# Optimization experiments

Hardware: AMD Instinct MI355X
Metric: run time of the kernel (lower is better)

## Reference

```python
import jax, jax.numpy as jnp
import numpy as np

FFT_LEN = 256
BATCH = 65536


def _dft_kernels():
    n = np.arange(FFT_LEN)
    k = n.reshape(-1, 1)
    cos_k = np.cos(2 * np.pi * k * n / FFT_LEN).astype(np.float32)   # [K, N]
    sin_k = (-np.sin(2 * np.pi * k * n / FFT_LEN)).astype(np.float32)  # [K, N], note the minus sign
    return jnp.asarray(cos_k), jnp.asarray(sin_k)


def setup_inputs() -> dict:
    key = jax.random.key(0)
    x = jax.random.normal(key, (BATCH, 2, FFT_LEN), dtype=jnp.float32)
    cos_kernel, sin_kernel = _dft_kernels()
    return {"x": x, "cos_kernel": cos_kernel, "sin_kernel": sin_kernel}


def reference(x, cos_kernel, sin_kernel):
    # x: [B, 2, 256] -> real/imag channels. Conv1d(kernel=256, no pad) over L=256
    # is exactly a dense 256x256 matmul per channel (a direct O(n^2) DFT).
    x_real = x[:, 0, :]  # [B, 256]
    x_imag = x[:, 1, :]  # [B, 256]
    # real_conv(v) = cos_kernel @ v ; imag_conv(v) = sin_kernel @ v
    real_part = jnp.einsum('kn,bn->bk', cos_kernel, x_real) - jnp.einsum('kn,bn->bk', sin_kernel, x_imag)
    imag_part = jnp.einsum('kn,bn->bk', cos_kernel, x_imag) + jnp.einsum('kn,bn->bk', sin_kernel, x_real)
    out = jnp.concatenate([real_part, imag_part], axis=1)  # [B, 512]
    return out[:, :, None]  # [B, 512, 1] matches torch conv output length 1
```

## Files before the change

### kernel.cpp

```cpp
#include <hip/hip_runtime.h>
#include <hip/hip_bf16.h>
#include <stdint.h>


typedef __attribute__((ext_vector_type(8))) short bf16x8;
typedef __attribute__((ext_vector_type(4))) float f32x4;

#define KDIM 512
#define NDIM 512
#define BM 64

__device__ __forceinline__ ushort f2bf(float f) {
  union { float f; uint32_t u; } v; v.f = f;
  uint32_t r = (v.u + 0x7fffu + ((v.u >> 16) & 1u)) >> 16;
  return (ushort)r;
}

__global__ __launch_bounds__(512) void build_w_kernel(const float* __restrict__ cosk,
                                                      const float* __restrict__ sink,
                                                      ushort* __restrict__ Wf) {
  int g = blockIdx.x * 512 + threadIdx.x;
  int lane = g & 63;
  int nt = (g >> 6) & 31;
  int j = nt * 16 + (lane & 15);
  int kbase = (g >> 11) * 32 + (lane >> 4) * 8;
  bf16x8 w8;
#pragma unroll
  for (int e = 0; e < 8; ++e) {
    int k = kbase + e;
    float v;
    if (j < 256) {
      v = (k < 256) ? cosk[(j << 8) + k] : -sink[(j << 8) + (k - 256)];
    } else {
      int jj = j - 256;
      v = (k < 256) ? sink[(jj << 8) + k] : cosk[(jj << 8) + (k - 256)];
    }
    w8[e] = (short)f2bf(v);
  }
  *reinterpret_cast<bf16x8*>(Wf + (size_t)g * 8) = w8;
}

__device__ __forceinline__ bf16x8 cvt8(f32x4 a, f32x4 b) {
  bf16x8 w8;
  w8[0] = (short)f2bf(a[0]); w8[1] = (short)f2bf(a[1]);
  w8[2] = (short)f2bf(a[2]); w8[3] = (short)f2bf(a[3]);
  w8[4] = (short)f2bf(b[0]); w8[5] = (short)f2bf(b[1]);
  w8[6] = (short)f2bf(b[2]); w8[7] = (short)f2bf(b[3]);
  return w8;
}

__global__ __launch_bounds__(512) void dft_gemm_kernel(const float* __restrict__ A,
                                                       const ushort* __restrict__ Wf,
                                                       float* __restrict__ out) {
  __shared__ ushort As[2][BM * 64];

  const int tid  = threadIdx.x;
  const int lane = tid & 63;
  const int wid  = tid >> 6;
  const int m0   = blockIdx.x * BM;
  const int c0   = wid * 64;

  const int srow = tid >> 3;
  const int skq  = (tid & 7) * 8;
  const float* ap = A + (size_t)(m0 + srow) * KDIM + skq;
  const int swidx = (srow << 6) + (skq ^ ((srow & 7) << 3));

  const int lrow = lane & 15;
  const int lk8  = (lane >> 4) * 8;

  const ushort* wp = Wf + (size_t)(c0 >> 4) * 512 + lane * 8;

  f32x4 acc[4][4] = {};

  f32x4 q0 = *reinterpret_cast<const f32x4*>(ap);
  f32x4 q1 = *reinterpret_cast<const f32x4*>(ap + 4);
  f32x4 p0 = *reinterpret_cast<const f32x4*>(ap + 64);
  f32x4 p1 = *reinterpret_cast<const f32x4*>(ap + 68);
  *reinterpret_cast<bf16x8*>(&As[0][swidx]) = cvt8(q0, q1);
  asm volatile("s_waitcnt lgkmcnt(0)" ::: "memory");
  __builtin_amdgcn_s_barrier();

#pragma unroll
  for (int t = 0; t < 8; ++t) {
    if (t < 7)
      *reinterpret_cast<bf16x8*>(&As[(t + 1) & 1][swidx]) = cvt8(p0, p1);

    bf16x8 wfr[2][4];
#pragma unroll
    for (int kk = 0; kk < 2; ++kk)
#pragma unroll
      for (int mi = 0; mi < 4; ++mi)
        wfr[kk][mi] = *reinterpret_cast<const bf16x8*>(
            wp + (size_t)((t * 2 + kk) * 32 + mi) * 512);

    if (t < 6) {
      p0 = *reinterpret_cast<const f32x4*>(ap + (t + 2) * 64);
      p1 = *reinterpret_cast<const f32x4*>(ap + (t + 2) * 64 + 4);
    }

#pragma unroll
    for (int kk = 0; kk < 2; ++kk) {
      bf16x8 xfr[4];
#pragma unroll
      for (int ni = 0; ni < 4; ++ni) {
        int row = ni * 16 + lrow;
        int idx = (row << 6) + ((kk * 32 + lk8) ^ ((lrow & 7) << 3));
        xfr[ni] = *reinterpret_cast<const bf16x8*>(&As[t & 1][idx]);
      }
#pragma unroll
      for (int mi = 0; mi < 4; ++mi)
#pragma unroll
        for (int ni = 0; ni < 4; ++ni)
          acc[mi][ni] = __builtin_amdgcn_mfma_f32_16x16x32_bf16(
              wfr[kk][mi], xfr[ni], acc[mi][ni], 0, 0, 0);
    }

    if (t < 7) {
      asm volatile("s_waitcnt lgkmcnt(0)" ::: "memory");
      __builtin_amdgcn_s_barrier();
    }
  }

  const int jbase = c0 + (lane >> 4) * 4;
#pragma unroll
  for (int ni = 0; ni < 4; ++ni) {
    size_t rowb = (size_t)(m0 + ni * 16 + lrow) * NDIM;
#pragma unroll
    for (int mi = 0; mi < 4; ++mi)
      *reinterpret_cast<f32x4*>(out + rowb + jbase + mi * 16) = acc[mi][ni];
  }
}

extern "C" void kernel_launch(void* const* d_in, const int* in_sizes, int n_in,
                              void* d_out, int out_size, void* d_ws, size_t ws_size,
                              hipStream_t stream) {
  const float* x    = (const float*)d_in[0];
  const float* cosk = (const float*)d_in[1];
  const float* sink = (const float*)d_in[2];
  float* out = (float*)d_out;
  ushort* Wf = (ushort*)d_ws;

  build_w_kernel<<<64, 512, 0, stream>>>(cosk, sink, Wf);
  dft_gemm_kernel<<<65536 / BM, 512, 0, stream>>>(x, Wf, out);
}
```

Baseline: 72.74 us.

## Stage activations in two half-K LDS phases instead of a double-buffered loop

Replaces the 8-step double-buffered LDS pipeline with two phases. Each phase loads four K-slices of the input at once, converts them to bf16 into a larger LDS buffer, syncs once, then runs four MFMA steps. This cuts the per-step barriers from seven to two and puts more global loads in flight together. LDS use grows from 16KB to 64KB per block, and the added launch-bound hint of 4 blocks per CU may not be reachable at that LDS size. It also gives up overlapping the load of the second half with compute on the first.

```diff
diff --git a/kernel.cpp b/kernel.cpp
--- a/kernel.cpp
+++ b/kernel.cpp
@@ -49,10 +49,10 @@
   return w8;
 }
 
-__global__ __launch_bounds__(512) void dft_gemm_kernel(const float* __restrict__ A,
-                                                       const ushort* __restrict__ Wf,
-                                                       float* __restrict__ out) {
-  __shared__ ushort As[2][BM * 64];
+__global__ __launch_bounds__(512, 4) void dft_gemm_kernel(const float* __restrict__ A,
+                                                          const ushort* __restrict__ Wf,
+                                                          float* __restrict__ out) {
+  __shared__ ushort As[8][64 * 64];
 
   const int tid  = threadIdx.x;
   const int lane = tid & 63;
@@ -63,7 +63,7 @@
   const int srow = tid >> 3;
   const int skq  = (tid & 7) * 8;
   const float* ap = A + (size_t)(m0 + srow) * KDIM + skq;
-  const int swidx = (srow << 6) + (skq ^ ((srow & 7) << 3));
+  const int swb = (srow << 6) + (skq ^ ((srow & 7) << 3));
 
   const int lrow = lane & 15;
   const int lk8  = (lane >> 4) * 8;
@@ -72,19 +72,22 @@
 
   f32x4 acc[4][4] = {};
 
-  f32x4 q0 = *reinterpret_cast<const f32x4*>(ap);
-  f32x4 q1 = *reinterpret_cast<const f32x4*>(ap + 4);
-  f32x4 p0 = *reinterpret_cast<const f32x4*>(ap + 64);
-  f32x4 p1 = *reinterpret_cast<const f32x4*>(ap + 68);
-  *reinterpret_cast<bf16x8*>(&As[0][swidx]) = cvt8(q0, q1);
+  {
+    f32x4 s[8];
+#pragma unroll
+    for (int t = 0; t < 4; ++t) {
+      s[2 * t]     = *reinterpret_cast<const f32x4*>(ap + t * 64);
+      s[2 * t + 1] = *reinterpret_cast<const f32x4*>(ap + t * 64 + 4);
+    }
+#pragma unroll
+    for (int t = 0; t < 4; ++t)
+      *reinterpret_cast<bf16x8*>(&As[t][swb]) = cvt8(s[2 * t], s[2 * t + 1]);
+  }
   asm volatile("s_waitcnt lgkmcnt(0)" ::: "memory");
   __builtin_amdgcn_s_barrier();
 
 #pragma unroll
-  for (int t = 0; t < 8; ++t) {
-    if (t < 7)
-      *reinterpret_cast<bf16x8*>(&As[(t + 1) & 1][swidx]) = cvt8(p0, p1);
-
+  for (int t = 0; t < 4; ++t) {
     bf16x8 wfr[2][4];
 #pragma unroll
     for (int kk = 0; kk < 2; ++kk)
@@ -92,12 +95,6 @@
       for (int mi = 0; mi < 4; ++mi)
         wfr[kk][mi] = *reinterpret_cast<const bf16x8*>(
             wp + (size_t)((t * 2 + kk) * 32 + mi) * 512);
-
-    if (t < 6) {
-      p0 = *reinterpret_cast<const f32x4*>(ap + (t + 2) * 64);
-      p1 = *reinterpret_cast<const f32x4*>(ap + (t + 2) * 64 + 4);
-    }
-
 #pragma unroll
     for (int kk = 0; kk < 2; ++kk) {
       bf16x8 xfr[4];
@@ -105,7 +102,7 @@
       for (int ni = 0; ni < 4; ++ni) {
         int row = ni * 16 + lrow;
         int idx = (row << 6) + ((kk * 32 + lk8) ^ ((lrow & 7) << 3));
-        xfr[ni] = *reinterpret_cast<const bf16x8*>(&As[t & 1][idx]);
+        xfr[ni] = *reinterpret_cast<const bf16x8*>(&As[t][idx]);
       }
 #pragma unroll
       for (int mi = 0; mi < 4; ++mi)
@@ -114,10 +111,46 @@
           acc[mi][ni] = __builtin_amdgcn_mfma_f32_16x16x32_bf16(
               wfr[kk][mi], xfr[ni], acc[mi][ni], 0, 0, 0);
     }
+  }
 
-    if (t < 7) {
-      asm volatile("s_waitcnt lgkmcnt(0)" ::: "memory");
-      __builtin_amdgcn_s_barrier();
+  {
+    f32x4 s[8];
+#pragma unroll
+    for (int t = 0; t < 4; ++t) {
+      s[2 * t]     = *reinterpret_cast<const f32x4*>(ap + (4 + t) * 64);
+      s[2 * t + 1] = *reinterpret_cast<const f32x4*>(ap + (4 + t) * 64 + 4);
+    }
+#pragma unroll
+    for (int t = 0; t < 4; ++t)
+      *reinterpret_cast<bf16x8*>(&As[4 + t][swb]) = cvt8(s[2 * t], s[2 * t + 1]);
+  }
+  asm volatile("s_waitcnt lgkmcnt(0)" ::: "memory");
+  __builtin_amdgcn_s_barrier();
+
+#pragma unroll
+  for (int t = 4; t < 8; ++t) {
+    bf16x8 wfr[2][4];
+#pragma unroll
+    for (int kk = 0; kk < 2; ++kk)
+#pragma unroll
+      for (int mi = 0; mi < 4; ++mi)
+        wfr[kk][mi] = *reinterpret_cast<const bf16x8*>(
+            wp + (size_t)((t * 2 + kk) * 32 + mi) * 512);
+#pragma unroll
+    for (int kk = 0; kk < 2; ++kk) {
+      bf16x8 xfr[4];
+#pragma unroll
+      for (int ni = 0; ni < 4; ++ni) {
+        int row = ni * 16 + lrow;
+        int idx = (row << 6) + ((kk * 32 + lk8) ^ ((lrow & 7) << 3));
+        xfr[ni] = *reinterpret_cast<const bf16x8*>(&As[t][idx]);
+      }
+#pragma unroll
+      for (int mi = 0; mi < 4; ++mi)
+#pragma unroll
+        for (int ni = 0; ni < 4; ++ni)
+          acc[mi][ni] = __builtin_amdgcn_mfma_f32_16x16x32_bf16(
+              wfr[kk][mi], xfr[ni], acc[mi][ni], 0, 0, 0);
     }
   }
 
```

Result: no change. 72.25 us (-0.7%).

## Double block M tile to 128 rows and software-pipeline weight fragment loads

Applied to the files above, without the earlier changes.

The row tile grows from 64 to 128, so each weight fragment fetched from global memory is reused across twice as many MFMA tiles, which halves weight traffic per output. Each thread now stages 16 floats per row chunk, and the x prefetch is moved to the top of each iteration, with the LDS store delayed to the end of the iteration. Weight fragments for the next k-half are loaded while the current half computes. The accumulator count doubles to 32 f32x4 per thread with launch_bounds(512,2), which raises register pressure and risks spills or lower occupancy.

```diff
diff --git a/kernel.cpp b/kernel.cpp
--- a/kernel.cpp
+++ b/kernel.cpp
@@ -8,7 +8,7 @@
 
 #define KDIM 512
 #define NDIM 512
-#define BM 64
+#define BM 128
 
 __device__ __forceinline__ ushort f2bf(float f) {
   union { float f; uint32_t u; } v; v.f = f;
@@ -49,9 +49,9 @@
   return w8;
 }
 
-__global__ __launch_bounds__(512) void dft_gemm_kernel(const float* __restrict__ A,
-                                                       const ushort* __restrict__ Wf,
-                                                       float* __restrict__ out) {
+__global__ __launch_bounds__(512, 2) void dft_gemm_kernel(const float* __restrict__ A,
+                                                          const ushort* __restrict__ Wf,
+                                                          float* __restrict__ out) {
   __shared__ ushort As[2][BM * 64];
 
   const int tid  = threadIdx.x;
@@ -60,62 +60,94 @@
   const int m0   = blockIdx.x * BM;
   const int c0   = wid * 64;
 
-  const int srow = tid >> 3;
-  const int skq  = (tid & 7) * 8;
+  const int srow  = tid >> 2;
+  const int skq   = (tid & 3) * 16;
   const float* ap = A + (size_t)(m0 + srow) * KDIM + skq;
-  const int swidx = (srow << 6) + (skq ^ ((srow & 7) << 3));
+  const int slot0 = (tid & 3) * 2;
+  const int eA = srow * 64 + (((slot0)     ^ (srow & 7)) << 3);
+  const int eB = srow * 64 + (((slot0 + 1) ^ (srow & 7)) << 3);
 
   const int lrow = lane & 15;
   const int lk8  = (lane >> 4) * 8;
 
   const ushort* wp = Wf + (size_t)(c0 >> 4) * 512 + lane * 8;
 
-  f32x4 acc[4][4] = {};
+  f32x4 acc[4][8] = {};
 
-  f32x4 q0 = *reinterpret_cast<const f32x4*>(ap);
-  f32x4 q1 = *reinterpret_cast<const f32x4*>(ap + 4);
-  f32x4 p0 = *reinterpret_cast<const f32x4*>(ap + 64);
-  f32x4 p1 = *reinterpret_cast<const f32x4*>(ap + 68);
-  *reinterpret_cast<bf16x8*>(&As[0][swidx]) = cvt8(q0, q1);
+  {
+    f32x4 s0 = *reinterpret_cast<const f32x4*>(ap);
+    f32x4 s1 = *reinterpret_cast<const f32x4*>(ap + 4);
+    f32x4 s2 = *reinterpret_cast<const f32x4*>(ap + 8);
+    f32x4 s3 = *reinterpret_cast<const f32x4*>(ap + 12);
+    *reinterpret_cast<bf16x8*>(&As[0][eA]) = cvt8(s0, s1);
+    *reinterpret_cast<bf16x8*>(&As[0][eB]) = cvt8(s2, s3);
+  }
+  bf16x8 wcur[4];
+#pragma unroll
+  for (int mi = 0; mi < 4; ++mi)
+    wcur[mi] = *reinterpret_cast<const bf16x8*>(wp + (size_t)mi * 512);
   asm volatile("s_waitcnt lgkmcnt(0)" ::: "memory");
   __builtin_amdgcn_s_barrier();
 
 #pragma unroll
   for (int t = 0; t < 8; ++t) {
-    if (t < 7)
-      *reinterpret_cast<bf16x8*>(&As[(t + 1) & 1][swidx]) = cvt8(p0, p1);
-
-    bf16x8 wfr[2][4];
-#pragma unroll
-    for (int kk = 0; kk < 2; ++kk)
-#pragma unroll
-      for (int mi = 0; mi < 4; ++mi)
-        wfr[kk][mi] = *reinterpret_cast<const bf16x8*>(
-            wp + (size_t)((t * 2 + kk) * 32 + mi) * 512);
-
-    if (t < 6) {
-      p0 = *reinterpret_cast<const f32x4*>(ap + (t + 2) * 64);
-      p1 = *reinterpret_cast<const f32x4*>(ap + (t + 2) * 64 + 4);
+    f32x4 x0, x1, x2, x3;
+    if (t < 7) {
+      const float* apn = ap + (t + 1) * 64;
+      x0 = *reinterpret_cast<const f32x4*>(apn);
+      x1 = *reinterpret_cast<const f32x4*>(apn + 4);
+      x2 = *reinterpret_cast<const f32x4*>(apn + 8);
+      x3 = *reinterpret_cast<const f32x4*>(apn + 12);
     }
 
+    bf16x8 wnxt[4];
 #pragma unroll
-    for (int kk = 0; kk < 2; ++kk) {
-      bf16x8 xfr[4];
+    for (int mi = 0; mi < 4; ++mi)
+      wnxt[mi] = *reinterpret_cast<const bf16x8*>(
+          wp + (size_t)((t * 2 + 1) * 32 + mi) * 512);
+
+    {
+      bf16x8 xfr[8];
 #pragma unroll
-      for (int ni = 0; ni < 4; ++ni) {
+      for (int ni = 0; ni < 8; ++ni) {
         int row = ni * 16 + lrow;
-        int idx = (row << 6) + ((kk * 32 + lk8) ^ ((lrow & 7) << 3));
+        int idx = (row << 6) + (lk8 ^ ((lrow & 7) << 3));
         xfr[ni] = *reinterpret_cast<const bf16x8*>(&As[t & 1][idx]);
       }
 #pragma unroll
       for (int mi = 0; mi < 4; ++mi)
 #pragma unroll
-        for (int ni = 0; ni < 4; ++ni)
+        for (int ni = 0; ni < 8; ++ni)
           acc[mi][ni] = __builtin_amdgcn_mfma_f32_16x16x32_bf16(
-              wfr[kk][mi], xfr[ni], acc[mi][ni], 0, 0, 0);
+              wcur[mi], xfr[ni], acc[mi][ni], 0, 0, 0);
     }
 
     if (t < 7) {
+#pragma unroll
+      for (int mi = 0; mi < 4; ++mi)
+        wcur[mi] = *reinterpret_cast<const bf16x8*>(
+            wp + (size_t)((t * 2 + 2) * 32 + mi) * 512);
+    }
+
+    {
+      bf16x8 xfr[8];
+#pragma unroll
+      for (int ni = 0; ni < 8; ++ni) {
+        int row = ni * 16 + lrow;
+        int idx = (row << 6) + ((32 + lk8) ^ ((lrow & 7) << 3));
+        xfr[ni] = *reinterpret_cast<const bf16x8*>(&As[t & 1][idx]);
+      }
+#pragma unroll
+      for (int mi = 0; mi < 4; ++mi)
+#pragma unroll
+        for (int ni = 0; ni < 8; ++ni)
+          acc[mi][ni] = __builtin_amdgcn_mfma_f32_16x16x32_bf16(
+              wnxt[mi], xfr[ni], acc[mi][ni], 0, 0, 0);
+    }
+
+    if (t < 7) {
+      *reinterpret_cast<bf16x8*>(&As[(t + 1) & 1][eA]) = cvt8(x0, x1);
+      *reinterpret_cast<bf16x8*>(&As[(t + 1) & 1][eB]) = cvt8(x2, x3);
       asm volatile("s_waitcnt lgkmcnt(0)" ::: "memory");
       __builtin_amdgcn_s_barrier();
     }
@@ -123,7 +155,7 @@
 
   const int jbase = c0 + (lane >> 4) * 4;
 #pragma unroll
-  for (int ni = 0; ni < 4; ++ni) {
+  for (int ni = 0; ni < 8; ++ni) {
     size_t rowb = (size_t)(m0 + ni * 16 + lrow) * NDIM;
 #pragma unroll
     for (int mi = 0; mi < 4; ++mi)
```

New measurement: 70.24 us. 3.4% less time.

## Load fp32 input directly into LDS and convert to bf16 at fragment read

Applied to the files above, without the earlier changes.

Replaces the register-staged path (global load, bf16 convert, LDS store) with direct global-to-LDS loads of raw fp32 data into a triple-buffered, swizzled shared tile. Conversion to bf16 now happens when each wave reads its MFMA fragments. This removes register staging and the explicit LDS store, and lets loads run further ahead. The cost is double the LDS footprint and read bandwidth, and conversion work repeated across all eight waves. Inside the loop the barrier no longer has an explicit vmcnt wait, so correctness depends on the compiler inserting the right wait for the LDS DMA.

```diff
diff --git a/kernel.cpp b/kernel.cpp
--- a/kernel.cpp
+++ b/kernel.cpp
@@ -40,6 +40,12 @@
   *reinterpret_cast<bf16x8*>(Wf + (size_t)g * 8) = w8;
 }
 
+__device__ __forceinline__ void gload_lds16(const float* g, float* l) {
+  __builtin_amdgcn_global_load_lds(
+      (__attribute__((address_space(1))) const void*)g,
+      (__attribute__((address_space(3))) void*)l, 16, 0, 0);
+}
+
 __device__ __forceinline__ bf16x8 cvt8(f32x4 a, f32x4 b) {
   bf16x8 w8;
   w8[0] = (short)f2bf(a[0]); w8[1] = (short)f2bf(a[1]);
@@ -52,7 +58,7 @@
 __global__ __launch_bounds__(512) void dft_gemm_kernel(const float* __restrict__ A,
                                                        const ushort* __restrict__ Wf,
                                                        float* __restrict__ out) {
-  __shared__ ushort As[2][BM * 64];
+  __shared__ float Xs[3][BM * 64];
 
   const int tid  = threadIdx.x;
   const int lane = tid & 63;
@@ -60,31 +66,30 @@
   const int m0   = blockIdx.x * BM;
   const int c0   = wid * 64;
 
-  const int srow = tid >> 3;
-  const int skq  = (tid & 7) * 8;
-  const float* ap = A + (size_t)(m0 + srow) * KDIM + skq;
-  const int swidx = (srow << 6) + (skq ^ ((srow & 7) << 3));
+  const int r0 = wid * 8 + (lane >> 4);
+  const int r1 = r0 + 4;
+  const int slin = (lane & 15) >> 1;
+  const int h4   = (lane & 1) << 2;
+  const float* g0 = A + (size_t)(m0 + r0) * KDIM + (((slin ^ (r0 & 7)) << 3) + h4);
+  const float* g1 = A + (size_t)(m0 + r1) * KDIM + (((slin ^ (r1 & 7)) << 3) + h4);
 
   const int lrow = lane & 15;
-  const int lk8  = (lane >> 4) * 8;
+  const int g16  = lane >> 4;
 
   const ushort* wp = Wf + (size_t)(c0 >> 4) * 512 + lane * 8;
 
   f32x4 acc[4][4] = {};
 
-  f32x4 q0 = *reinterpret_cast<const f32x4*>(ap);
-  f32x4 q1 = *reinterpret_cast<const f32x4*>(ap + 4);
-  f32x4 p0 = *reinterpret_cast<const f32x4*>(ap + 64);
-  f32x4 p1 = *reinterpret_cast<const f32x4*>(ap + 68);
-  *reinterpret_cast<bf16x8*>(&As[0][swidx]) = cvt8(q0, q1);
-  asm volatile("s_waitcnt lgkmcnt(0)" ::: "memory");
+  gload_lds16(g0,      &Xs[0][wid * 512]);
+  gload_lds16(g1,      &Xs[0][wid * 512 + 256]);
+  gload_lds16(g0 + 64, &Xs[1][wid * 512]);
+  gload_lds16(g1 + 64, &Xs[1][wid * 512 + 256]);
+  asm volatile("s_waitcnt vmcnt(2)" ::: "memory");
+  __builtin_amdgcn_sched_barrier(0);
   __builtin_amdgcn_s_barrier();
 
 #pragma unroll
   for (int t = 0; t < 8; ++t) {
-    if (t < 7)
-      *reinterpret_cast<bf16x8*>(&As[(t + 1) & 1][swidx]) = cvt8(p0, p1);
-
     bf16x8 wfr[2][4];
 #pragma unroll
     for (int kk = 0; kk < 2; ++kk)
@@ -94,8 +99,8 @@
             wp + (size_t)((t * 2 + kk) * 32 + mi) * 512);
 
     if (t < 6) {
-      p0 = *reinterpret_cast<const f32x4*>(ap + (t + 2) * 64);
-      p1 = *reinterpret_cast<const f32x4*>(ap + (t + 2) * 64 + 4);
+      gload_lds16(g0 + (t + 2) * 64, &Xs[(t + 2) % 3][wid * 512]);
+      gload_lds16(g1 + (t + 2) * 64, &Xs[(t + 2) % 3][wid * 512 + 256]);
     }
 
 #pragma unroll
@@ -104,8 +109,11 @@
 #pragma unroll
       for (int ni = 0; ni < 4; ++ni) {
         int row = ni * 16 + lrow;
-        int idx = (row << 6) + ((kk * 32 + lk8) ^ ((lrow & 7) << 3));
-        xfr[ni] = *reinterpret_cast<const bf16x8*>(&As[t & 1][idx]);
+        int s = kk * 4 + g16;
+        const float* p = &Xs[t % 3][(row << 6) + ((s ^ (row & 7)) << 3)];
+        f32x4 a = *reinterpret_cast<const f32x4*>(p);
+        f32x4 b = *reinterpret_cast<const f32x4*>(p + 4);
+        xfr[ni] = cvt8(a, b);
       }
 #pragma unroll
       for (int mi = 0; mi < 4; ++mi)
@@ -116,7 +124,7 @@
     }
 
     if (t < 7) {
-      asm volatile("s_waitcnt lgkmcnt(0)" ::: "memory");
+      __builtin_amdgcn_sched_barrier(0);
       __builtin_amdgcn_s_barrier();
     }
   }
```

Measured after the change: 107.0 us. 47.1% more time.
